# Kernel tuning notes

Hardware: AMD Instinct MI355X
Metric: run time of the kernel (lower is better)

Reference implementation:

```python
import jax, jax.numpy as jnp
import numpy as np

B, N, DIN = 8, 50000, 16
E, M, CH = 800000, 25000, 64
C_HALF = CH // 2


def setup_inputs() -> dict:
    key = jax.random.key(0)
    ks = jax.random.split(key, 9)
    x = jax.random.normal(ks[0], (B, N, DIN), dtype=jnp.float32)
    adj_rows = jax.random.randint(ks[1], (E,), 0, N, dtype=jnp.int32)
    adj_cols = jax.random.randint(ks[2], (E,), 0, N, dtype=jnp.int32)
    adj_vals = jax.random.uniform(ks[3], (E,), dtype=jnp.float32)
    centroids = jax.random.randint(ks[4], (M,), 0, N, dtype=jnp.int32)
    # Conv1d(kernel_size=1) weights == dense [out, in] matrices
    W_lin = jax.random.normal(ks[5], (C_HALF, DIN), dtype=jnp.float32) * (1.0 / np.sqrt(DIN))
    b_lin = jax.random.normal(ks[6], (C_HALF,), dtype=jnp.float32) * 0.01
    W_eye = jax.random.normal(ks[7], (C_HALF, DIN), dtype=jnp.float32) * (1.0 / np.sqrt(DIN))
    b_eye = jax.random.normal(ks[8], (C_HALF,), dtype=jnp.float32) * 0.01
    return {"x": x, "adj_rows": adj_rows, "adj_cols": adj_cols, "adj_vals": adj_vals,
            "centroids": centroids, "W_lin": W_lin, "b_lin": b_lin,
            "W_eye": W_eye, "b_eye": b_eye}


def reference(x, adj_rows, adj_cols, adj_vals, centroids, W_lin, b_lin, W_eye, b_eye):
    # x: [B, N, DIN] -> permute to channels-first [B, DIN, N]
    xc = jnp.transpose(x, (0, 2, 1))
    # eye branch: 1x1 conv == pointwise linear over channel dim
    eye_x = jnp.einsum('bcn,oc->bon', xc, W_eye) + b_eye[None, :, None]  # [B, C/2, N]
    # SpMM aggregation: adj @ x.T where x is [B*DIN, N]
    xt = xc.reshape(-1, xc.shape[-1]).T                      # [N, B*DIN]
    msgs = adj_vals[:, None] * xt[adj_cols]                  # [E, B*DIN] gather
    agg = jax.ops.segment_sum(msgs, adj_rows, num_segments=xt.shape[0])  # [N, B*DIN] scatter-add
    xa = agg.T.reshape(xc.shape)                             # [B, DIN, N]
    lin_x = jnp.einsum('bcn,oc->bon', xa, W_lin) + b_lin[None, :, None]  # [B, C/2, N]
    out = jax.nn.relu(jnp.concatenate([lin_x, eye_x], axis=1))  # [B, C, N]
    out = out[:, :, centroids]                               # gather centroid nodes [B, C, M]
    return jnp.transpose(out, (0, 2, 1))                     # [B, M, C]
```

## Files before the change

kernel.cpp:

```cpp
#include <hip/hip_runtime.h>

#define DIN   16
#define BB    8
#define FDIM  128
#define CHALF 32
#define CH    64
#define CAP   52
#define CAP2  16

__device__ __forceinline__ unsigned bf16rne(float f) {
    unsigned u = __float_as_uint(f);
    return (u + 0x7FFFu + ((u >> 16) & 1u)) >> 16;
}

__global__ __launch_bounds__(256) void prep_kernel(
    const float4* __restrict__ x4, uint2* __restrict__ xt2, int N, int nbT,
    const int* __restrict__ centroids, int* __restrict__ seen,
    int* __restrict__ rankid, int* __restrict__ active_list,
    int* __restrict__ nactive, int* __restrict__ cnt2, int* __restrict__ mlist,
    int M) {
    if (blockIdx.x < (unsigned)nbT) {
        int i = blockIdx.x * 256 + threadIdx.x;
        int n = i >> 5, slot = i & 31, b = slot >> 2, q = slot & 3;
        float4 v = x4[((long long)b * N + n) * 4 + q];
        uint2 o;
        o.x = bf16rne(v.x) | (bf16rne(v.y) << 16);
        o.y = bf16rne(v.z) | (bf16rne(v.w) << 16);
        xt2[i] = o;
    } else {
        int t = (blockIdx.x - nbT) * 256 + threadIdx.x;
        if (t >= M) return;
        int n = centroids[t];
        if (atomicExch(&seen[n], 1) == 0) {
            int r = atomicAdd(nactive, 1);
            rankid[n] = r + 1;
            active_list[r] = n;
        }
        int pos = atomicAdd(&cnt2[n], 1);
        if (pos < CAP2) mlist[n * CAP2 + pos] = t;
    }
}

__global__ __launch_bounds__(256) void bin_kernel(
    const int* __restrict__ rows, const int* __restrict__ cols,
    const float* __restrict__ vals, const int* __restrict__ rankid,
    int* __restrict__ cnt, int2* __restrict__ bins, int E) {
    int idx = blockIdx.x * blockDim.x + threadIdx.x;
    int e0 = idx * 2;
    if (e0 >= E) return;
    int2   r2 = ((const int2*)rows)[idx];
    int2   c2 = ((const int2*)cols)[idx];
    float2 v2 = ((const float2*)vals)[idx];
    int rr0 = rankid[r2.x];
    if (rr0 != 0) {
        int a = rr0 - 1;
        int pos = atomicAdd(&cnt[a], 1);
        if (pos < CAP)
            bins[(long long)a * CAP + pos] = make_int2(c2.x, __float_as_int(v2.x));
    }
    if (e0 + 1 < E) {
        int rr1 = rankid[r2.y];
        if (rr1 != 0) {
            int a = rr1 - 1;
            int pos = atomicAdd(&cnt[a], 1);
            if (pos < CAP)
                bins[(long long)a * CAP + pos] = make_int2(c2.y, __float_as_int(v2.y));
        }
    }
}

__global__ __launch_bounds__(256) void gather_kernel(
    const uint2* __restrict__ xt2, const int* __restrict__ cnt,
    const int2* __restrict__ bins, const int* __restrict__ active_list,
    const int* __restrict__ nactive,
    const int* __restrict__ cnt2, const int* __restrict__ mlist,
    const float* __restrict__ W_lin, const float* __restrict__ b_lin,
    const float* __restrict__ W_eye, const float* __restrict__ b_eye,
    float* __restrict__ out, int M) {
    if (blockIdx.x * 4 >= (unsigned)*nactive) return;

    int tid = threadIdx.x;
    int w = tid >> 6;
    int l = tid & 63;

    __shared__ float sWc[DIN][CH + 1];
    __shared__ float sb[CH];
    __shared__ float sagg[4][FDIM];
    __shared__ float sx[4][FDIM];

    #pragma unroll
    for (int i = tid; i < CH * DIN; i += 256) {
        int o = i >> 4, cc = i & 15;
        sWc[cc][o] = (o < CHALF) ? W_lin[i] : W_eye[i - CHALF * DIN];
    }
    if (tid < CHALF) sb[tid] = b_lin[tid];
    else if (tid < CH) sb[tid] = b_eye[tid - CHALF];
    __syncthreads();

    int a = blockIdx.x * 4 + w;
    if (a >= *nactive) return;
    int n = active_list[a];
    int c = min(cnt[a], CAP);

    int g = l >> 5;
    int s = l & 31;

    int2 myedge = make_int2(0, 0);
    if (l < c) myedge = bins[(long long)a * CAP + l];
    uint2 xraw = make_uint2(0u, 0u);
    if (g == 0) xraw = xt2[(long long)n * 32 + s];

    int iters = (c + 7) >> 3;
    float4 acc = make_float4(0.f, 0.f, 0.f, 0.f);
    for (int i = 0; i < iters; ++i) {
        int k0 = 8 * i + g;
        int k1 = k0 + 2;
        int k2 = k0 + 4;
        int k3 = k0 + 6;
        int   col0 = __shfl(myedge.x, k0);
        float v0   = __int_as_float(__shfl(myedge.y, k0));
        int   col1 = __shfl(myedge.x, k1);
        float v1   = __int_as_float(__shfl(myedge.y, k1));
        int   col2 = __shfl(myedge.x, k2);
        float v2   = __int_as_float(__shfl(myedge.y, k2));
        int   col3 = __shfl(myedge.x, k3);
        float v3   = __int_as_float(__shfl(myedge.y, k3));
        uint2 u0 = xt2[(long long)col0 * 32 + s];
        uint2 u1 = xt2[(long long)col1 * 32 + s];
        uint2 u2 = xt2[(long long)col2 * 32 + s];
        uint2 u3 = xt2[(long long)col3 * 32 + s];
        acc.x += v0 * __uint_as_float(u0.x << 16);
        acc.y += v0 * __uint_as_float(u0.x & 0xFFFF0000u);
        acc.z += v0 * __uint_as_float(u0.y << 16);
        acc.w += v0 * __uint_as_float(u0.y & 0xFFFF0000u);
        acc.x += v1 * __uint_as_float(u1.x << 16);
        acc.y += v1 * __uint_as_float(u1.x & 0xFFFF0000u);
        acc.z += v1 * __uint_as_float(u1.y << 16);
        acc.w += v1 * __uint_as_float(u1.y & 0xFFFF0000u);
        acc.x += v2 * __uint_as_float(u2.x << 16);
        acc.y += v2 * __uint_as_float(u2.x & 0xFFFF0000u);
        acc.z += v2 * __uint_as_float(u2.y << 16);
        acc.w += v2 * __uint_as_float(u2.y & 0xFFFF0000u);
        acc.x += v3 * __uint_as_float(u3.x << 16);
        acc.y += v3 * __uint_as_float(u3.x & 0xFFFF0000u);
        acc.z += v3 * __uint_as_float(u3.y << 16);
        acc.w += v3 * __uint_as_float(u3.y & 0xFFFF0000u);
    }
    acc.x += __shfl_xor(acc.x, 32);
    acc.y += __shfl_xor(acc.y, 32);
    acc.z += __shfl_xor(acc.z, 32);
    acc.w += __shfl_xor(acc.w, 32);
    if (g == 0) {
        ((float4*)sagg[w])[s] = acc;
        float4 xr;
        xr.x = __uint_as_float(xraw.x << 16);
        xr.y = __uint_as_float(xraw.x & 0xFFFF0000u);
        xr.z = __uint_as_float(xraw.y << 16);
        xr.w = __uint_as_float(xraw.y & 0xFFFF0000u);
        ((float4*)sx[w])[s] = xr;
    }

    int o = l;
    float wreg[DIN];
    #pragma unroll
    for (int cc = 0; cc < DIN; ++cc) wreg[cc] = sWc[cc][o];
    const float* src = (o < CHALF) ? sagg[w] : sx[w];
    float bias = sb[o];
    float res[BB];
    #pragma unroll
    for (int b = 0; b < BB; ++b) {
        float r = bias;
        #pragma unroll
        for (int cc = 0; cc < DIN; ++cc) r += wreg[cc] * src[b * DIN + cc];
        res[b] = fmaxf(r, 0.f);
    }

    int nm = min(cnt2[n], CAP2);
    for (int mm = 0; mm < nm; ++mm) {
        int m = mlist[n * CAP2 + mm];
        float* dst = out + (long long)m * CH + o;
        #pragma unroll
        for (int b = 0; b < BB; ++b)
            dst[(long long)b * M * CH] = res[b];
    }
}

extern "C" void kernel_launch(void* const* d_in, const int* in_sizes, int n_in,
                              void* d_out, int out_size, void* d_ws, size_t ws_size,
                              hipStream_t stream) {
    const float* x        = (const float*)d_in[0];
    const int*   adj_rows = (const int*)d_in[1];
    const int*   adj_cols = (const int*)d_in[2];
    const float* adj_vals = (const float*)d_in[3];
    const int*   cents    = (const int*)d_in[4];
    const float* W_lin    = (const float*)d_in[5];
    const float* b_lin    = (const float*)d_in[6];
    const float* W_eye    = (const float*)d_in[7];
    const float* b_eye    = (const float*)d_in[8];
    float* out = (float*)d_out;

    const int E = in_sizes[1];
    const int M = in_sizes[4];
    const int N = in_sizes[0] / (BB * DIN);

    char* p = (char*)d_ws;
    uint2* xt2   = (uint2*)p;   p += (size_t)N * 32 * sizeof(uint2);
    int2*  bins  = (int2*)p;    p += (size_t)M * CAP * sizeof(int2);
    int*   mlist = (int*)p;     p += (size_t)N * CAP2 * sizeof(int);
    int*   alist = (int*)p;     p += (size_t)M * sizeof(int);
    char* zbase = p;
    int* seen    = (int*)p;     p += (size_t)N * sizeof(int);
    int* rankid  = (int*)p;     p += (size_t)N * sizeof(int);
    int* cnt     = (int*)p;     p += (size_t)M * sizeof(int);
    int* cnt2    = (int*)p;     p += (size_t)N * sizeof(int);
    int* nactive = (int*)p;     p += 16 * sizeof(int);
    size_t zbytes = (size_t)(p - zbase);

    hipMemsetAsync(zbase, 0, zbytes, stream);

    int nbT = (N * 32) / 256;
    int nbM = (M + 255) / 256;
    prep_kernel<<<nbT + nbM, 256, 0, stream>>>((const float4*)x, xt2, N, nbT,
                                               cents, seen, rankid, alist,
                                               nactive, cnt2, mlist, M);

    bin_kernel<<<(E / 2 + 255) / 256, 256, 0, stream>>>(adj_rows, adj_cols, adj_vals,
                                                        rankid, cnt, bins, E);

    int gblocks = (M + 3) / 4;
    gather_kernel<<<gblocks, 256, 0, stream>>>(xt2, cnt, bins, alist, nactive,
                                               cnt2, mlist,
                                               W_lin, b_lin, W_eye, b_eye, out, M);
}
```

Before: 155.1 us.

## Bin all edges by node index and fuse binning into prep kernel

Edges are now binned by their destination node directly, with no rank lookup, so binning no longer depends on the centroid-ranking pass. This lets binning, the bf16 transpose and centroid registration run as block ranges of one launch, removing a kernel boundary and the dependent rankid gather. In exchange every edge now does an atomic and a scattered write, including edges to nodes that are never centroids (roughly half of them). The bins buffer and counters grow to N entries, so there is more memset and write traffic.

```diff
diff --git a/kernel.cpp b/kernel.cpp
--- a/kernel.cpp
+++ b/kernel.cpp
@@ -14,13 +14,33 @@
 }
 
 __global__ __launch_bounds__(256) void prep_kernel(
-    const float4* __restrict__ x4, uint2* __restrict__ xt2, int N, int nbT,
+    const float4* __restrict__ x4, uint2* __restrict__ xt2, int N,
+    int nbB, int nbT,
+    const int* __restrict__ rows, const int* __restrict__ cols,
+    const float* __restrict__ vals, int* __restrict__ cnt,
+    int2* __restrict__ bins, int E,
     const int* __restrict__ centroids, int* __restrict__ seen,
-    int* __restrict__ rankid, int* __restrict__ active_list,
-    int* __restrict__ nactive, int* __restrict__ cnt2, int* __restrict__ mlist,
-    int M) {
-    if (blockIdx.x < (unsigned)nbT) {
-        int i = blockIdx.x * 256 + threadIdx.x;
+    int* __restrict__ active_list, int* __restrict__ nactive,
+    int* __restrict__ cnt2, int* __restrict__ mlist, int M) {
+    if (blockIdx.x < (unsigned)nbB) {
+        int idx = blockIdx.x * 256 + threadIdx.x;
+        int e0 = idx * 2;
+        if (e0 >= E) return;
+        int2   r2 = ((const int2*)rows)[idx];
+        int2   c2 = ((const int2*)cols)[idx];
+        float2 v2 = ((const float2*)vals)[idx];
+        {
+            int pos = atomicAdd(&cnt[r2.x], 1);
+            if (pos < CAP)
+                bins[(long long)r2.x * CAP + pos] = make_int2(c2.x, __float_as_int(v2.x));
+        }
+        if (e0 + 1 < E) {
+            int pos = atomicAdd(&cnt[r2.y], 1);
+            if (pos < CAP)
+                bins[(long long)r2.y * CAP + pos] = make_int2(c2.y, __float_as_int(v2.y));
+        }
+    } else if (blockIdx.x < (unsigned)(nbB + nbT)) {
+        int i = (blockIdx.x - nbB) * 256 + threadIdx.x;
         int n = i >> 5, slot = i & 31, b = slot >> 2, q = slot & 3;
         float4 v = x4[((long long)b * N + n) * 4 + q];
         uint2 o;
@@ -28,44 +48,15 @@
         o.y = bf16rne(v.z) | (bf16rne(v.w) << 16);
         xt2[i] = o;
     } else {
-        int t = (blockIdx.x - nbT) * 256 + threadIdx.x;
+        int t = (blockIdx.x - nbB - nbT) * 256 + threadIdx.x;
         if (t >= M) return;
         int n = centroids[t];
         if (atomicExch(&seen[n], 1) == 0) {
             int r = atomicAdd(nactive, 1);
-            rankid[n] = r + 1;
             active_list[r] = n;
         }
         int pos = atomicAdd(&cnt2[n], 1);
         if (pos < CAP2) mlist[n * CAP2 + pos] = t;
-    }
-}
-
-__global__ __launch_bounds__(256) void bin_kernel(
-    const int* __restrict__ rows, const int* __restrict__ cols,
-    const float* __restrict__ vals, const int* __restrict__ rankid,
-    int* __restrict__ cnt, int2* __restrict__ bins, int E) {
-    int idx = blockIdx.x * blockDim.x + threadIdx.x;
-    int e0 = idx * 2;
-    if (e0 >= E) return;
-    int2   r2 = ((const int2*)rows)[idx];
-    int2   c2 = ((const int2*)cols)[idx];
-    float2 v2 = ((const float2*)vals)[idx];
-    int rr0 = rankid[r2.x];
-    if (rr0 != 0) {
-        int a = rr0 - 1;
-        int pos = atomicAdd(&cnt[a], 1);
-        if (pos < CAP)
-            bins[(long long)a * CAP + pos] = make_int2(c2.x, __float_as_int(v2.x));
-    }
-    if (e0 + 1 < E) {
-        int rr1 = rankid[r2.y];
-        if (rr1 != 0) {
-            int a = rr1 - 1;
-            int pos = atomicAdd(&cnt[a], 1);
-            if (pos < CAP)
-                bins[(long long)a * CAP + pos] = make_int2(c2.y, __float_as_int(v2.y));
-        }
     }
 }
 
@@ -100,13 +91,13 @@
     int a = blockIdx.x * 4 + w;
     if (a >= *nactive) return;
     int n = active_list[a];
-    int c = min(cnt[a], CAP);
+    int c = min(cnt[n], CAP);
 
     int g = l >> 5;
     int s = l & 31;
 
     int2 myedge = make_int2(0, 0);
-    if (l < c) myedge = bins[(long long)a * CAP + l];
+    if (l < c) myedge = bins[(long long)n * CAP + l];
     uint2 xraw = make_uint2(0u, 0u);
     if (g == 0) xraw = xt2[(long long)n * 32 + s];
 
@@ -205,27 +196,25 @@
 
     char* p = (char*)d_ws;
     uint2* xt2   = (uint2*)p;   p += (size_t)N * 32 * sizeof(uint2);
-    int2*  bins  = (int2*)p;    p += (size_t)M * CAP * sizeof(int2);
+    int2*  bins  = (int2*)p;    p += (size_t)N * CAP * sizeof(int2);
     int*   mlist = (int*)p;     p += (size_t)N * CAP2 * sizeof(int);
     int*   alist = (int*)p;     p += (size_t)M * sizeof(int);
     char* zbase = p;
     int* seen    = (int*)p;     p += (size_t)N * sizeof(int);
-    int* rankid  = (int*)p;     p += (size_t)N * sizeof(int);
-    int* cnt     = (int*)p;     p += (size_t)M * sizeof(int);
+    int* cnt     = (int*)p;     p += (size_t)N * sizeof(int);
     int* cnt2    = (int*)p;     p += (size_t)N * sizeof(int);
     int* nactive = (int*)p;     p += 16 * sizeof(int);
     size_t zbytes = (size_t)(p - zbase);
 
     hipMemsetAsync(zbase, 0, zbytes, stream);
 
+    int nbB = (E / 2 + 255) / 256;
     int nbT = (N * 32) / 256;
     int nbM = (M + 255) / 256;
-    prep_kernel<<<nbT + nbM, 256, 0, stream>>>((const float4*)x, xt2, N, nbT,
-                                               cents, seen, rankid, alist,
-                                               nactive, cnt2, mlist, M);
-
-    bin_kernel<<<(E / 2 + 255) / 256, 256, 0, stream>>>(adj_rows, adj_cols, adj_vals,
-                                                        rankid, cnt, bins, E);
+    prep_kernel<<<nbB + nbT + nbM, 256, 0, stream>>>(
+        (const float4*)x, xt2, N, nbB, nbT,
+        adj_rows, adj_cols, adj_vals, cnt, bins, E,
+        cents, seen, alist, nactive, cnt2, mlist, M);
 
     int gblocks = (M + 3) / 4;
     gather_kernel<<<gblocks, 256, 0, stream>>>(xt2, cnt, bins, alist, nactive,
```

After: 188.4 us. 1.21x slower.
